# Performance work log

Measured on AMD Instinct MI355X. Metric: run time of the kernel, lower is better.

## Reference

```python
import jax, jax.numpy as jnp
import numpy as np

N, E = 50000, 800000
D_IN, HID, HEADS, D_OUT = 128, 32, 4, 40
NEG_SLOPE = 0.2
BN_EPS = 1e-5


def gat_conv(x, src, dst, W, a_src, a_dst, b, heads, ch):
    """PyG-style GATConv (eval mode, self-loops already appended to src/dst)."""
    n = x.shape[0]
    h = (x @ W).reshape(n, heads, ch)                      # [N,H,C]
    al_src = jnp.einsum('nhc,hc->nh', h, a_src)            # [N,H]
    al_dst = jnp.einsum('nhc,hc->nh', h, a_dst)
    e = jax.nn.leaky_relu(al_src[src] + al_dst[dst], NEG_SLOPE)  # [Etot,H]
    # segment softmax over incoming edges of each dst node
    e_max = jax.ops.segment_max(e, dst, num_segments=n)
    e = jnp.exp(e - e_max[dst])
    denom = jax.ops.segment_sum(e, dst, num_segments=n)
    alpha = e / (denom[dst] + 1e-16)                        # [Etot,H]
    msg = h[src] * alpha[:, :, None]                        # [Etot,H,C]
    out = jax.ops.segment_sum(msg, dst, num_segments=n)     # [N,H,C]
    return out.reshape(n, heads * ch) + b


def bn_eval(x, g, b, m, v):
    return (x - m) * jax.lax.rsqrt(v + BN_EPS) * g + b


def setup_inputs() -> dict:
    key = jax.random.key(0)
    ks = jax.random.split(key, 24)
    p = lambda k, s: jax.random.normal(k, s, jnp.float32) * 0.1
    inp = {
        'x': jax.random.normal(ks[0], (N, D_IN), jnp.float32),
        'edge_index': jax.random.randint(ks[1], (2, E), 0, N),
        'W1': p(ks[2], (D_IN, HEADS * HID)),
        'a_src1': p(ks[3], (HEADS, HID)), 'a_dst1': p(ks[4], (HEADS, HID)),
        'b1': jnp.zeros((HEADS * HID,), jnp.float32),
        'W2': p(ks[5], (HEADS * HID, HEADS * HID)),
        'a_src2': p(ks[6], (HEADS, HID)), 'a_dst2': p(ks[7], (HEADS, HID)),
        'b2': jnp.zeros((HEADS * HID,), jnp.float32),
        'W3': p(ks[8], (HEADS * HID, D_OUT)),
        'a_src3': p(ks[9], (1, D_OUT)), 'a_dst3': p(ks[10], (1, D_OUT)),
        'b3': jnp.zeros((D_OUT,), jnp.float32),
        'bn1_g': jnp.ones((HEADS * HID,), jnp.float32),
        'bn1_b': jnp.zeros((HEADS * HID,), jnp.float32),
        'bn1_m': p(ks[11], (HEADS * HID,)),
        'bn1_v': jax.random.uniform(ks[12], (HEADS * HID,), jnp.float32) + 0.5,
        'bn2_g': jnp.ones((HEADS * HID,), jnp.float32),
        'bn2_b': jnp.zeros((HEADS * HID,), jnp.float32),
        'bn2_m': p(ks[13], (HEADS * HID,)),
        'bn2_v': jax.random.uniform(ks[14], (HEADS * HID,), jnp.float32) + 0.5,
    }
    return inp


def reference(x, edge_index, W1, a_src1, a_dst1, b1, W2, a_src2, a_dst2, b2,
              W3, a_src3, a_dst3, b3, bn1_g, bn1_b, bn1_m, bn1_v,
              bn2_g, bn2_b, bn2_m, bn2_v):
    n = x.shape[0]
    loop = jnp.arange(n, dtype=edge_index.dtype)
    src = jnp.concatenate([edge_index[0], loop])   # add self loops (PyG default)
    dst = jnp.concatenate([edge_index[1], loop])

    h = gat_conv(x, src, dst, W1, a_src1, a_dst1, b1, HEADS, HID)
    h = jax.nn.relu(h)
    h = bn_eval(h, bn1_g, bn1_b, bn1_m, bn1_v)      # dropout = identity (eval)

    h = gat_conv(h, src, dst, W2, a_src2, a_dst2, b2, HEADS, HID)
    h = jax.nn.relu(h)
    h = bn_eval(h, bn2_g, bn2_b, bn2_m, bn2_v)

    h = gat_conv(h, src, dst, W3, a_src3, a_dst3, b3, 1, D_OUT)
    return jax.nn.log_softmax(h, axis=1)
```

## Files before the change

kernel.cpp:

```cpp
#include <hip/hip_runtime.h>
#include <hip/hip_bf16.h>
#include <math.h>

using bf16 = __hip_bfloat16;
using frag8 = __attribute__((ext_vector_type(8))) short;
using f32x4 = __attribute__((ext_vector_type(4))) float;

#define LEAKY 0.2f
#define BN_EPS 1e-5f
#define NEGBIG -1e30f

__device__ __forceinline__ float lrelu(float z){ return z > 0.f ? z : LEAKY * z; }
__device__ __forceinline__ float bflo(unsigned u){ return __uint_as_float(u << 16); }
__device__ __forceinline__ float bfhi(unsigned u){ return __uint_as_float(u & 0xffff0000u); }
__device__ __forceinline__ unsigned pk(float a, float b){
  unsigned ua = __float_as_uint(a), ub = __float_as_uint(b);
  ua += 0x7fffu + ((ua >> 16) & 1u);
  ub += 0x7fffu + ((ub >> 16) & 1u);
  return (ua >> 16) | (ub & 0xffff0000u);
}
__device__ __forceinline__ float ldf(const void* p, size_t i, int isbf){
  if (isbf) return (float)((const bf16*)p)[i];
  return ((const float*)p)[i];
}

union U4F8 { uint4 u; frag8 f; };

__device__ __forceinline__ frag8 load_a_pairs(const unsigned* __restrict__ X2, int node, int k0){
  U4F8 v; v.u = *((const uint4*)(X2 + (size_t)node*64 + (k0 >> 1))); return v.f;
}
__device__ __forceinline__ frag8 load_a_f32(const float* __restrict__ X, int node, int k0){
  float4 q0 = *((const float4*)(X + (size_t)node*128 + k0));
  float4 q1 = *((const float4*)(X + (size_t)node*128 + k0 + 4));
  U4F8 v; v.u = make_uint4(pk(q0.x,q0.y), pk(q0.z,q0.w), pk(q1.x,q1.y), pk(q1.z,q1.w));
  return v.f;
}

__global__ void init_detect(int* head, const unsigned short* __restrict__ w1bits,
                            int* flag, int n){
  int g = blockIdx.x*256 + threadIdx.x;
  if (g < n) head[g] = -1;
  if (blockIdx.x == 0){
    __shared__ int cntr;
    if (threadIdx.x == 0) cntr = 0;
    __syncthreads();
    unsigned u = w1bits[threadIdx.x * 2];
    int e = (u >> 7) & 0xff;
    atomicAdd(&cntr, (e >= 64 && e <= 140) ? 1 : 0);
    __syncthreads();
    if (threadIdx.x == 0) *flag = (cntr >= 160) ? 1 : 0;
  }
}

__global__ void chain_build(const int* __restrict__ dst, int* head, int* next,
                            int e, int n){
  int g = blockIdx.x*256 + threadIdx.x;
  if (g < e){
    int d = dst[g];
    next[g] = ((unsigned)d < (unsigned)n) ? atomicExch(&head[d], g) : -1;
  }
}

__global__ void chain_count(const int* __restrict__ head, const int* __restrict__ next,
                            int* cnt, int* total, int n){
  int g = blockIdx.x*256 + threadIdx.x;
  if (g == 0) *total = 0;
  if (g >= n) return;
  int c = 0;
  for (int e = head[g]; e != -1; e = next[e]) ++c;
  cnt[g] = c;
}

__global__ void csr_scan(const int* __restrict__ cnt, int* start, int* total, int n){
  __shared__ int s[256];
  __shared__ int base_s;
  int t = threadIdx.x;
  int g = blockIdx.x*256 + t;
  int v = (g < n) ? cnt[g] : 0;
  s[t] = v;
  __syncthreads();
  for (int off = 1; off < 256; off <<= 1){
    int x = (t >= off) ? s[t-off] : 0;
    __syncthreads();
    s[t] += x;
    __syncthreads();
  }
  if (t == 255) base_s = atomicAdd(total, s[255]);
  __syncthreads();
  if (g < n) start[g] = base_s + s[t] - v;
}

__global__ void chain_fill(const int* __restrict__ head, const int* __restrict__ next,
                           const int* __restrict__ src, const int* __restrict__ start,
                           int* col, int n){
  int g = blockIdx.x*256 + threadIdx.x;
  if (g >= n) return;
  int p = start[g];
  for (int e = head[g]; e != -1; e = next[e])
    col[p++] = src[e];
}

__global__ __launch_bounds__(256) void gemm_al_mfma(
    const void* __restrict__ X, int xkind,
    const void* __restrict__ W, const void* __restrict__ Wsrc, const void* __restrict__ Wdst,
    const int* __restrict__ flagp,
    unsigned* __restrict__ H2, float* __restrict__ AL, float* __restrict__ AD,
    int n, int ntiles)
{
  __shared__ unsigned short WT[128*136];
  const int isbf = *flagp;
  const int t = threadIdx.x;
  if (isbf){
    const unsigned short* W16 = (const unsigned short*)W;
    for (int idx = t; idx < 16384; idx += 256){
      int k = idx >> 7, nn = idx & 127;
      WT[nn*136 + k] = W16[idx];
    }
  } else {
    const float* Wf = (const float*)W;
    for (int idx = t; idx < 16384; idx += 256){
      int k = idx >> 7, nn = idx & 127;
      WT[nn*136 + k] = (unsigned short)(pk(Wf[idx], 0.f) & 0xffffu);
    }
  }
  __syncthreads();
  const int w = t >> 6;
  const int lane = t & 63;
  const int m = lane & 15, quad = lane >> 4;

  frag8 bf[4][2];
  #pragma unroll
  for (int s = 0; s < 4; ++s)
    #pragma unroll
    for (int ct = 0; ct < 2; ++ct){
      int colc = w*32 + ct*16 + m;
      int k0 = s*32 + quad*8;
      U4F8 v; v.u = *((const uint4*)&WT[colc*136 + k0]);
      bf[s][ct] = v.f;
    }
  float avv[2], dvv[2];
  #pragma unroll
  for (int ct = 0; ct < 2; ++ct){
    int colc = w*32 + ct*16 + m;
    avv[ct] = ldf(Wsrc, colc, isbf);
    dvv[ct] = ldf(Wdst, colc, isbf);
  }
  const bool pairs = (xkind == 1) || isbf;

  for (int tile = blockIdx.x; tile < ntiles; tile += gridDim.x){
    const int mb = tile*16;
    int nodeA = mb + m; if (nodeA >= n) nodeA = n - 1;
    frag8 af[4];
    #pragma unroll
    for (int s = 0; s < 4; ++s){
      int k0 = s*32 + quad*8;
      af[s] = pairs ? load_a_pairs((const unsigned*)X, nodeA, k0)
                    : load_a_f32((const float*)X, nodeA, k0);
    }
    f32x4 acc0 = {0.f,0.f,0.f,0.f}, acc1 = {0.f,0.f,0.f,0.f};
    #pragma unroll
    for (int s = 0; s < 4; ++s){
      acc0 = __builtin_amdgcn_mfma_f32_16x16x32_bf16(af[s], bf[s][0], acc0, 0,0,0);
      acc1 = __builtin_amdgcn_mfma_f32_16x16x32_bf16(af[s], bf[s][1], acc1, 0,0,0);
    }
    #pragma unroll
    for (int r = 0; r < 4; ++r){
      int g = mb + quad*4 + r;
      float v0 = acc0[r], v1 = acc1[r];
      unsigned u0 = pk(v0, __shfl_xor(v0, 1));
      unsigned u1 = pk(v1, __shfl_xor(v1, 1));
      bool ok = g < n;
      if (((lane & 1) == 0) && ok){
        H2[(size_t)g*64 + w*16 + (m >> 1)]     = u0;
        H2[(size_t)g*64 + w*16 + 8 + (m >> 1)] = u1;
      }
      float s1 = v0*avv[0] + v1*avv[1];
      float s2 = v0*dvv[0] + v1*dvv[1];
      s1 += __shfl_xor(s1,1); s1 += __shfl_xor(s1,2); s1 += __shfl_xor(s1,4); s1 += __shfl_xor(s1,8);
      s2 += __shfl_xor(s2,1); s2 += __shfl_xor(s2,2); s2 += __shfl_xor(s2,4); s2 += __shfl_xor(s2,8);
      if (m == 0 && ok){ AL[g*4 + w] = s1; AD[g*4 + w] = s2; }
    }
  }
}

__global__ __launch_bounds__(256) void gemm3_mfma(
    const unsigned* __restrict__ X2, const void* __restrict__ W,
    const void* __restrict__ Wsrc, const void* __restrict__ Wdst,
    const int* __restrict__ flagp,
    unsigned* __restrict__ H3, float* __restrict__ AL, float* __restrict__ AD,
    int n, int ntiles)
{
  __shared__ unsigned short WT[48*136];
  const int isbf = *flagp;
  const int t = threadIdx.x;
  for (int idx = t; idx < 128*64; idx += 256){
    int c = idx & 63, k = idx >> 6;
    if (c < 48){
      unsigned short v = 0;
      if (c < 40){
        if (isbf) v = ((const unsigned short*)W)[k*40 + c];
        else      v = (unsigned short)(pk(((const float*)W)[k*40 + c], 0.f) & 0xffffu);
      }
      WT[c*136 + k] = v;
    }
  }
  __syncthreads();
  const int w = t >> 6;
  const int lane = t & 63;
  const int m = lane & 15, quad = lane >> 4;

  frag8 bf[4][3];
  float avv[3], dvv[3];
  #pragma unroll
  for (int ct = 0; ct < 3; ++ct){
    int colc = ct*16 + m;
    #pragma unroll
    for (int s = 0; s < 4; ++s){
      int k0 = s*32 + quad*8;
      U4F8 v; v.u = *((const uint4*)&WT[colc*136 + k0]);
      bf[s][ct] = v.f;
    }
    avv[ct] = (colc < 40) ? ldf(Wsrc, colc, isbf) : 0.f;
    dvv[ct] = (colc < 40) ? ldf(Wdst, colc, isbf) : 0.f;
  }

  for (int tg = blockIdx.x; tg*4 < ntiles; tg += gridDim.x){
    const int tile = tg*4 + w;
    if (tile >= ntiles) continue;
    const int mb = tile*16;
    int nodeA = mb + m; if (nodeA >= n) nodeA = n - 1;
    frag8 af[4];
    #pragma unroll
    for (int s = 0; s < 4; ++s)
      af[s] = load_a_pairs(X2, nodeA, s*32 + quad*8);
    f32x4 acc[3];
    #pragma unroll
    for (int ct = 0; ct < 3; ++ct) acc[ct] = (f32x4){0.f,0.f,0.f,0.f};
    #pragma unroll
    for (int s = 0; s < 4; ++s){
      acc[0] = __builtin_amdgcn_mfma_f32_16x16x32_bf16(af[s], bf[s][0], acc[0], 0,0,0);
      acc[1] = __builtin_amdgcn_mfma_f32_16x16x32_bf16(af[s], bf[s][1], acc[1], 0,0,0);
      acc[2] = __builtin_amdgcn_mfma_f32_16x16x32_bf16(af[s], bf[s][2], acc[2], 0,0,0);
    }
    #pragma unroll
    for (int r = 0; r < 4; ++r){
      int g = mb + quad*4 + r;
      bool ok = g < n;
      float ps = 0.f, pd = 0.f;
      #pragma unroll
      for (int ct = 0; ct < 3; ++ct){
        float v = acc[ct][r];
        ps += v*avv[ct]; pd += v*dvv[ct];
        unsigned u = pk(v, __shfl_xor(v, 1));
        bool stok = ((lane & 1) == 0) && ok && (ct < 2 || m < 8);
        if (stok) H3[(size_t)g*20 + ct*8 + (m >> 1)] = u;
      }
      ps += __shfl_xor(ps,1); ps += __shfl_xor(ps,2); ps += __shfl_xor(ps,4); ps += __shfl_xor(ps,8);
      pd += __shfl_xor(pd,1); pd += __shfl_xor(pd,2); pd += __shfl_xor(pd,4); pd += __shfl_xor(pd,8);
      if (m == 0 && ok){ AL[g] = ps; AD[g] = pd; }
    }
  }
}

__global__ __launch_bounds__(256) void agg4(
    const unsigned* __restrict__ H2,
    const float* __restrict__ ALf, const float* __restrict__ ADf,
    const int* __restrict__ cnt, const int* __restrict__ start, const int* __restrict__ col,
    const void* __restrict__ bias, const void* __restrict__ bng, const void* __restrict__ bnb,
    const void* __restrict__ bnm,  const void* __restrict__ bnv,
    const int* __restrict__ flagp,
    unsigned* __restrict__ Hout, int n)
{
  const int isbf = *flagp;
  const int wave = threadIdx.x >> 6;
  const int lane = threadIdx.x & 63;
  const int node = blockIdx.x*4 + wave;
  if (node >= n) return;
  const int head = lane >> 4;
  const float ad = ADf[node*4 + head];
  const int base = start[node], deg = cnt[node];

  float accL, accH, l;
  {
    float e = __expf(lrelu(ALf[node*4 + head] + ad));
    unsigned h = H2[(size_t)node*64 + lane];
    l = e; accL = e * bflo(h); accH = e * bfhi(h);
  }

  int i = 0;
  for (; i + 8 <= deg; i += 8){
    int sv[8]; float av[8]; unsigned hv[8];
    #pragma unroll
    for (int u = 0; u < 8; ++u){
      int s = col[base + i + u];
      sv[u] = ((unsigned)s < (unsigned)n) ? s : 0;
    }
    #pragma unroll
    for (int u = 0; u < 8; ++u) av[u] = ALf[sv[u]*4 + head];
    #pragma unroll
    for (int u = 0; u < 8; ++u) hv[u] = H2[(size_t)sv[u]*64 + lane];
    #pragma unroll
    for (int u = 0; u < 8; ++u){
      float e = __expf(lrelu(av[u] + ad));
      l    += e;
      accL += e * bflo(hv[u]);
      accH += e * bfhi(hv[u]);
    }
  }
  for (; i < deg; ++i){
    int s = col[base + i];
    if ((unsigned)s >= (unsigned)n) s = 0;
    float a = ALf[s*4 + head];
    unsigned h = H2[(size_t)s*64 + lane];
    float e = __expf(lrelu(a + ad));
    l += e; accL += e * bflo(h); accH += e * bfhi(h);
  }

  const float rl = 1.f / l;
  const int c0 = 2*lane, c1 = c0 + 1;
  float v0 = fmaxf(accL*rl + ldf(bias,c0,isbf), 0.f);
  v0 = (v0 - ldf(bnm,c0,isbf)) * rsqrtf(ldf(bnv,c0,isbf) + BN_EPS) * ldf(bng,c0,isbf) + ldf(bnb,c0,isbf);
  float v1 = fmaxf(accH*rl + ldf(bias,c1,isbf), 0.f);
  v1 = (v1 - ldf(bnm,c1,isbf)) * rsqrtf(ldf(bnv,c1,isbf) + BN_EPS) * ldf(bng,c1,isbf) + ldf(bnb,c1,isbf);
  Hout[(size_t)node*64 + lane] = pk(v0, v1);
}

__global__ __launch_bounds__(256) void agg1(
    const unsigned* __restrict__ H3,
    const float* __restrict__ AL, const float* __restrict__ AD,
    const int* __restrict__ cnt, const int* __restrict__ start, const int* __restrict__ col,
    const void* __restrict__ b3, const int* __restrict__ flagp,
    void* __restrict__ out, int n)
{
  const int isbf = *flagp;
  const int wave = threadIdx.x >> 6;
  const int lane = threadIdx.x & 63;
  const int node = blockIdx.x*4 + wave;
  if (node >= n) return;
  const float ad = AD[node];
  const bool act = lane < 20;
  const int base = start[node], deg = cnt[node];

  float accL, accH, l;
  {
    float e = __expf(lrelu(AL[node] + ad));
    unsigned h = act ? H3[(size_t)node*20 + lane] : 0u;
    l = e; accL = e * bflo(h); accH = e * bfhi(h);
  }

  int i = 0;
  for (; i + 8 <= deg; i += 8){
    int sv[8]; float av[8]; unsigned hv[8];
    #pragma unroll
    for (int u = 0; u < 8; ++u){
      int s = col[base + i + u];
      sv[u] = ((unsigned)s < (unsigned)n) ? s : 0;
    }
    #pragma unroll
    for (int u = 0; u < 8; ++u) av[u] = AL[sv[u]];
    #pragma unroll
    for (int u = 0; u < 8; ++u) hv[u] = act ? H3[(size_t)sv[u]*20 + lane] : 0u;
    #pragma unroll
    for (int u = 0; u < 8; ++u){
      float e = __expf(lrelu(av[u] + ad));
      l    += e;
      accL += e * bflo(hv[u]);
      accH += e * bfhi(hv[u]);
    }
  }
  for (; i < deg; ++i){
    int s = col[base + i];
    if ((unsigned)s >= (unsigned)n) s = 0;
    float a = AL[s];
    unsigned h = act ? H3[(size_t)s*20 + lane] : 0u;
    float e = __expf(lrelu(a + ad));
    l += e; accL += e * bflo(h); accH += e * bfhi(h);
  }

  const float rl = 1.f / l;
  const int c0 = 2*lane;
  float z0 = act ? (accL*rl + ldf(b3, c0,     isbf)) : NEGBIG;
  float z1 = act ? (accH*rl + ldf(b3, c0 + 1, isbf)) : NEGBIG;
  float mx = fmaxf(z0, z1);
  #pragma unroll
  for (int off = 1; off < 64; off <<= 1) mx = fmaxf(mx, __shfl_xor(mx, off));
  float p = act ? (__expf(z0 - mx) + __expf(z1 - mx)) : 0.f;
  float sum = p;
  #pragma unroll
  for (int off = 1; off < 64; off <<= 1) sum += __shfl_xor(sum, off);
  if (act){
    float lg = __logf(sum);
    float r0 = z0 - mx - lg, r1 = z1 - mx - lg;
    if (isbf) ((unsigned*)out)[(size_t)node*20 + lane] = pk(r0, r1);
    else      ((float2*)out)[(size_t)node*20 + lane] = make_float2(r0, r1);
  }
}

extern "C" void kernel_launch(void* const* d_in, const int* in_sizes, int n_in,
                              void* d_out, int out_size, void* d_ws, size_t ws_size,
                              hipStream_t stream)
{
  (void)n_in; (void)out_size; (void)ws_size;
  const void* x    = d_in[0];
  const int*  ei   = (const int*)d_in[1];
  const void* W1   = d_in[2];
  const void* as1  = d_in[3];
  const void* ad1  = d_in[4];
  const void* b1   = d_in[5];
  const void* W2   = d_in[6];
  const void* as2  = d_in[7];
  const void* ad2  = d_in[8];
  const void* b2   = d_in[9];
  const void* W3   = d_in[10];
  const void* as3  = d_in[11];
  const void* ad3  = d_in[12];
  const void* b3   = d_in[13];
  const void* bn1g = d_in[14];
  const void* bn1b = d_in[15];
  const void* bn1m = d_in[16];
  const void* bn1v = d_in[17];
  const void* bn2g = d_in[18];
  const void* bn2b = d_in[19];
  const void* bn2m = d_in[20];
  const void* bn2v = d_in[21];

  const int N  = in_sizes[0] / 128;
  const int E  = in_sizes[1] / 2;
  const int ntiles = (N + 15) / 16;

  char* w = (char*)d_ws;
  size_t off = 0;
  auto alloc = [&](size_t bytes)->char*{
    char* p = w + off; off = (off + bytes + 255) & ~(size_t)255; return p;
  };
  unsigned* H2A = (unsigned*)alloc((size_t)N*64*4);
  unsigned* H2B = (unsigned*)alloc((size_t)N*64*4);
  unsigned* H3p = (unsigned*)alloc((size_t)N*20*4);
  float* AL   = (float*)alloc((size_t)N*4*4);
  float* AD   = (float*)alloc((size_t)N*4*4);
  int*   headp = (int*)alloc((size_t)N*4);
  int*   nextp = (int*)alloc((size_t)E*4);
  int*   cnt   = (int*)alloc((size_t)N*4);
  int*   start = (int*)alloc((size_t)N*4);
  int*   col   = (int*)alloc((size_t)E*4);
  int*   flag  = (int*)alloc(256);
  int*   total = (int*)alloc(256);

  const int* srcp = ei;
  const int* dstp = ei + E;

  const int nb256 = (N + 255)/256, eb256 = (E + 255)/256;
  const int bb = (N + 3)/4;
  int g1 = ntiles < 625 ? ntiles : 625;
  int g3 = (ntiles + 3)/4; if (g3 > 400) g3 = 400;

  init_detect<<<nb256,256,0,stream>>>(headp, (const unsigned short*)W1, flag, N);
  chain_build<<<eb256,256,0,stream>>>(dstp, headp, nextp, E, N);
  chain_count<<<nb256,256,0,stream>>>(headp, nextp, cnt, total, N);
  csr_scan  <<<nb256,256,0,stream>>>(cnt, start, total, N);
  chain_fill<<<nb256,256,0,stream>>>(headp, nextp, srcp, start, col, N);

  gemm_al_mfma<<<g1,256,0,stream>>>(x, 0, W1, as1, ad1, flag, H2A, AL, AD, N, ntiles);
  agg4<<<bb,256,0,stream>>>(H2A, AL, AD, cnt, start, col,
                            b1, bn1g, bn1b, bn1m, bn1v, flag, H2B, N);
  gemm_al_mfma<<<g1,256,0,stream>>>(H2B, 1, W2, as2, ad2, flag, H2A, AL, AD, N, ntiles);
  agg4<<<bb,256,0,stream>>>(H2A, AL, AD, cnt, start, col,
                            b2, bn2g, bn2b, bn2m, bn2v, flag, H2B, N);
  gemm3_mfma<<<g3,256,0,stream>>>(H2B, W3, as3, ad3, flag, H3p, AL, AD, N, ntiles);
  agg1<<<bb,256,0,stream>>>(H3p, AL, AD, cnt, start, col, b3, flag, d_out, N);
}
```

Baseline: 384.4 us.

## Build CSR via histogram+scatter and pack more nodes per wave in aggregation

```diff
diff --git a/kernel.cpp b/kernel.cpp
--- a/kernel.cpp
+++ b/kernel.cpp
@@ -10,7 +10,7 @@
 #define BN_EPS 1e-5f
 #define NEGBIG -1e30f
 
-__device__ __forceinline__ float lrelu(float z){ return z > 0.f ? z : LEAKY * z; }
+__device__ __forceinline__ float lrelu(float z){ return fmaxf(z, LEAKY * z); }
 __device__ __forceinline__ float bflo(unsigned u){ return __uint_as_float(u << 16); }
 __device__ __forceinline__ float bfhi(unsigned u){ return __uint_as_float(u & 0xffff0000u); }
 __device__ __forceinline__ unsigned pk(float a, float b){
@@ -36,10 +36,11 @@
   return v.f;
 }
 
-__global__ void init_detect(int* head, const unsigned short* __restrict__ w1bits,
-                            int* flag, int n){
+__global__ void init_detect(int* cnt, const unsigned short* __restrict__ w1bits,
+                            int* flag, int* total, int n){
   int g = blockIdx.x*256 + threadIdx.x;
-  if (g < n) head[g] = -1;
+  if (g < n) cnt[g] = 0;
+  if (g == 0) *total = 0;
   if (blockIdx.x == 0){
     __shared__ int cntr;
     if (threadIdx.x == 0) cntr = 0;
@@ -52,26 +53,16 @@
   }
 }
 
-__global__ void chain_build(const int* __restrict__ dst, int* head, int* next,
-                            int e, int n){
+__global__ void hist(const int* __restrict__ dst, int* cnt, int e, int n){
   int g = blockIdx.x*256 + threadIdx.x;
   if (g < e){
     int d = dst[g];
-    next[g] = ((unsigned)d < (unsigned)n) ? atomicExch(&head[d], g) : -1;
-  }
-}
-
-__global__ void chain_count(const int* __restrict__ head, const int* __restrict__ next,
-                            int* cnt, int* total, int n){
-  int g = blockIdx.x*256 + threadIdx.x;
-  if (g == 0) *total = 0;
-  if (g >= n) return;
-  int c = 0;
-  for (int e = head[g]; e != -1; e = next[e]) ++c;
-  cnt[g] = c;
-}
-
-__global__ void csr_scan(const int* __restrict__ cnt, int* start, int* total, int n){
+    if ((unsigned)d < (unsigned)n) atomicAdd(&cnt[d], 1);
+  }
+}
+
+__global__ void csr_scan(const int* __restrict__ cnt, int* start, int* pos,
+                         int* total, int n){
   __shared__ int s[256];
   __shared__ int base_s;
   int t = threadIdx.x;
@@ -87,17 +78,23 @@
   }
   if (t == 255) base_s = atomicAdd(total, s[255]);
   __syncthreads();
-  if (g < n) start[g] = base_s + s[t] - v;
-}
-
-__global__ void chain_fill(const int* __restrict__ head, const int* __restrict__ next,
-                           const int* __restrict__ src, const int* __restrict__ start,
-                           int* col, int n){
+  if (g < n){
+    int st = base_s + s[t] - v;
+    start[g] = st;
+    pos[g] = st;
+  }
+}
+
+__global__ void scatter(const int* __restrict__ src, const int* __restrict__ dst,
+                        int* pos, int* col, int e, int n){
   int g = blockIdx.x*256 + threadIdx.x;
-  if (g >= n) return;
-  int p = start[g];
-  for (int e = head[g]; e != -1; e = next[e])
-    col[p++] = src[e];
+  if (g < e){
+    int d = dst[g];
+    if ((unsigned)d < (unsigned)n){
+      int p = atomicAdd(&pos[d], 1);
+      col[p] = src[g];
+    }
+  }
 }
 
 __global__ __launch_bounds__(256) void gemm_al_mfma(
@@ -272,57 +269,73 @@
     unsigned* __restrict__ Hout, int n)
 {
   const int isbf = *flagp;
-  const int wave = threadIdx.x >> 6;
-  const int lane = threadIdx.x & 63;
-  const int node = blockIdx.x*4 + wave;
+  const int t = threadIdx.x;
+  const int grp = t >> 4;
+  const int p = t & 15;
+  const int node = blockIdx.x*16 + grp;
   if (node >= n) return;
-  const int head = lane >> 4;
+  const int head = p >> 2;
   const float ad = ADf[node*4 + head];
   const int base = start[node], deg = cnt[node];
 
-  float accL, accH, l;
+  float acc[8], l;
   {
     float e = __expf(lrelu(ALf[node*4 + head] + ad));
-    unsigned h = H2[(size_t)node*64 + lane];
-    l = e; accL = e * bflo(h); accH = e * bfhi(h);
+    uint4 h = *((const uint4*)(H2 + (size_t)node*64 + p*4));
+    l = e;
+    acc[0] = e*bflo(h.x); acc[1] = e*bfhi(h.x);
+    acc[2] = e*bflo(h.y); acc[3] = e*bfhi(h.y);
+    acc[4] = e*bflo(h.z); acc[5] = e*bfhi(h.z);
+    acc[6] = e*bflo(h.w); acc[7] = e*bfhi(h.w);
   }
 
   int i = 0;
-  for (; i + 8 <= deg; i += 8){
-    int sv[8]; float av[8]; unsigned hv[8];
-    #pragma unroll
-    for (int u = 0; u < 8; ++u){
+  for (; i + 4 <= deg; i += 4){
+    int sv[4]; float av[4]; uint4 hv[4];
+    #pragma unroll
+    for (int u = 0; u < 4; ++u){
       int s = col[base + i + u];
       sv[u] = ((unsigned)s < (unsigned)n) ? s : 0;
     }
     #pragma unroll
-    for (int u = 0; u < 8; ++u) av[u] = ALf[sv[u]*4 + head];
-    #pragma unroll
-    for (int u = 0; u < 8; ++u) hv[u] = H2[(size_t)sv[u]*64 + lane];
-    #pragma unroll
-    for (int u = 0; u < 8; ++u){
+    for (int u = 0; u < 4; ++u) av[u] = ALf[sv[u]*4 + head];
+    #pragma unroll
+    for (int u = 0; u < 4; ++u) hv[u] = *((const uint4*)(H2 + (size_t)sv[u]*64 + p*4));
+    #pragma unroll
+    for (int u = 0; u < 4; ++u){
       float e = __expf(lrelu(av[u] + ad));
-      l    += e;
-      accL += e * bflo(hv[u]);
-      accH += e * bfhi(hv[u]);
+      l += e;
+      acc[0] += e*bflo(hv[u].x); acc[1] += e*bfhi(hv[u].x);
+      acc[2] += e*bflo(hv[u].y); acc[3] += e*bfhi(hv[u].y);
+      acc[4] += e*bflo(hv[u].z); acc[5] += e*bfhi(hv[u].z);
+      acc[6] += e*bflo(hv[u].w); acc[7] += e*bfhi(hv[u].w);
     }
   }
   for (; i < deg; ++i){
     int s = col[base + i];
     if ((unsigned)s >= (unsigned)n) s = 0;
     float a = ALf[s*4 + head];
-    unsigned h = H2[(size_t)s*64 + lane];
+    uint4 h = *((const uint4*)(H2 + (size_t)s*64 + p*4));
     float e = __expf(lrelu(a + ad));
-    l += e; accL += e * bflo(h); accH += e * bfhi(h);
+    l += e;
+    acc[0] += e*bflo(h.x); acc[1] += e*bfhi(h.x);
+    acc[2] += e*bflo(h.y); acc[3] += e*bfhi(h.y);
+    acc[4] += e*bflo(h.z); acc[5] += e*bfhi(h.z);
+    acc[6] += e*bflo(h.w); acc[7] += e*bfhi(h.w);
   }
 
   const float rl = 1.f / l;
-  const int c0 = 2*lane, c1 = c0 + 1;
-  float v0 = fmaxf(accL*rl + ldf(bias,c0,isbf), 0.f);
-  v0 = (v0 - ldf(bnm,c0,isbf)) * rsqrtf(ldf(bnv,c0,isbf) + BN_EPS) * ldf(bng,c0,isbf) + ldf(bnb,c0,isbf);
-  float v1 = fmaxf(accH*rl + ldf(bias,c1,isbf), 0.f);
-  v1 = (v1 - ldf(bnm,c1,isbf)) * rsqrtf(ldf(bnv,c1,isbf) + BN_EPS) * ldf(bng,c1,isbf) + ldf(bnb,c1,isbf);
-  Hout[(size_t)node*64 + lane] = pk(v0, v1);
+  unsigned o[4];
+  #pragma unroll
+  for (int q = 0; q < 4; ++q){
+    const int c0 = p*8 + 2*q, c1 = c0 + 1;
+    float v0 = fmaxf(acc[2*q]*rl + ldf(bias,c0,isbf), 0.f);
+    v0 = (v0 - ldf(bnm,c0,isbf)) * rsqrtf(ldf(bnv,c0,isbf) + BN_EPS) * ldf(bng,c0,isbf) + ldf(bnb,c0,isbf);
+    float v1 = fmaxf(acc[2*q+1]*rl + ldf(bias,c1,isbf), 0.f);
+    v1 = (v1 - ldf(bnm,c1,isbf)) * rsqrtf(ldf(bnv,c1,isbf) + BN_EPS) * ldf(bng,c1,isbf) + ldf(bnb,c1,isbf);
+    o[q] = pk(v0, v1);
+  }
+  *((uint4*)(Hout + (size_t)node*64 + p*4)) = make_uint4(o[0], o[1], o[2], o[3]);
 }
 
 __global__ __launch_bounds__(256) void agg1(
@@ -333,35 +346,35 @@
     void* __restrict__ out, int n)
 {
   const int isbf = *flagp;
-  const int wave = threadIdx.x >> 6;
-  const int lane = threadIdx.x & 63;
-  const int node = blockIdx.x*4 + wave;
+  const int t = threadIdx.x;
+  const int p = t & 31;
+  const int node = blockIdx.x*8 + (t >> 5);
   if (node >= n) return;
   const float ad = AD[node];
-  const bool act = lane < 20;
+  const bool act = p < 20;
   const int base = start[node], deg = cnt[node];
 
   float accL, accH, l;
   {
     float e = __expf(lrelu(AL[node] + ad));
-    unsigned h = act ? H3[(size_t)node*20 + lane] : 0u;
+    unsigned h = act ? H3[(size_t)node*20 + p] : 0u;
     l = e; accL = e * bflo(h); accH = e * bfhi(h);
   }
 
   int i = 0;
-  for (; i + 8 <= deg; i += 8){
-    int sv[8]; float av[8]; unsigned hv[8];
-    #pragma unroll
-    for (int u = 0; u < 8; ++u){
+  for (; i + 4 <= deg; i += 4){
+    int sv[4]; float av[4]; unsigned hv[4];
+    #pragma unroll
+    for (int u = 0; u < 4; ++u){
       int s = col[base + i + u];
       sv[u] = ((unsigned)s < (unsigned)n) ? s : 0;
     }
     #pragma unroll
-    for (int u = 0; u < 8; ++u) av[u] = AL[sv[u]];
-    #pragma unroll
-    for (int u = 0; u < 8; ++u) hv[u] = act ? H3[(size_t)sv[u]*20 + lane] : 0u;
-    #pragma unroll
-    for (int u = 0; u < 8; ++u){
+    for (int u = 0; u < 4; ++u) av[u] = AL[sv[u]];
+    #pragma unroll
+    for (int u = 0; u < 4; ++u) hv[u] = act ? H3[(size_t)sv[u]*20 + p] : 0u;
+    #pragma unroll
+    for (int u = 0; u < 4; ++u){
       float e = __expf(lrelu(av[u] + ad));
       l    += e;
       accL += e * bflo(hv[u]);
@@ -372,27 +385,27 @@
     int s = col[base + i];
     if ((unsigned)s >= (unsigned)n) s = 0;
     float a = AL[s];
-    unsigned h = act ? H3[(size_t)s*20 + lane] : 0u;
+    unsigned h = act ? H3[(size_t)s*20 + p] : 0u;
     float e = __expf(lrelu(a + ad));
     l += e; accL += e * bflo(h); accH += e * bfhi(h);
   }
 
   const float rl = 1.f / l;
-  const int c0 = 2*lane;
+  const int c0 = 2*p;
   float z0 = act ? (accL*rl + ldf(b3, c0,     isbf)) : NEGBIG;
   float z1 = act ? (accH*rl + ldf(b3, c0 + 1, isbf)) : NEGBIG;
   float mx = fmaxf(z0, z1);
   #pragma unroll
-  for (int off = 1; off < 64; off <<= 1) mx = fmaxf(mx, __shfl_xor(mx, off));
-  float p = act ? (__expf(z0 - mx) + __expf(z1 - mx)) : 0.f;
-  float sum = p;
-  #pragma unroll
-  for (int off = 1; off < 64; off <<= 1) sum += __shfl_xor(sum, off);
+  for (int off = 1; off < 32; off <<= 1) mx = fmaxf(mx, __shfl_xor(mx, off));
+  float pp = act ? (__expf(z0 - mx) + __expf(z1 - mx)) : 0.f;
+  float sum = pp;
+  #pragma unroll
+  for (int off = 1; off < 32; off <<= 1) sum += __shfl_xor(sum, off);
   if (act){
     float lg = __logf(sum);
     float r0 = z0 - mx - lg, r1 = z1 - mx - lg;
-    if (isbf) ((unsigned*)out)[(size_t)node*20 + lane] = pk(r0, r1);
-    else      ((float2*)out)[(size_t)node*20 + lane] = make_float2(r0, r1);
+    if (isbf) ((unsigned*)out)[(size_t)node*20 + p] = pk(r0, r1);
+    else      ((float2*)out)[(size_t)node*20 + p] = make_float2(r0, r1);
   }
 }
 
@@ -438,10 +451,9 @@
   unsigned* H3p = (unsigned*)alloc((size_t)N*20*4);
   float* AL   = (float*)alloc((size_t)N*4*4);
   float* AD   = (float*)alloc((size_t)N*4*4);
-  int*   headp = (int*)alloc((size_t)N*4);
-  int*   nextp = (int*)alloc((size_t)E*4);
   int*   cnt   = (int*)alloc((size_t)N*4);
   int*   start = (int*)alloc((size_t)N*4);
+  int*   pos   = (int*)alloc((size_t)N*4);
   int*   col   = (int*)alloc((size_t)E*4);
   int*   flag  = (int*)alloc(256);
   int*   total = (int*)alloc(256);
@@ -450,22 +462,22 @@
   const int* dstp = ei + E;
 
   const int nb256 = (N + 255)/256, eb256 = (E + 255)/256;
-  const int bb = (N + 3)/4;
+  const int bb4 = (N + 15)/16;
+  const int bb1 = (N + 7)/8;
   int g1 = ntiles < 625 ? ntiles : 625;
   int g3 = (ntiles + 3)/4; if (g3 > 400) g3 = 400;
 
-  init_detect<<<nb256,256,0,stream>>>(headp, (const unsigned short*)W1, flag, N);
-  chain_build<<<eb256,256,0,stream>>>(dstp, headp, nextp, E, N);
-  chain_count<<<nb256,256,0,stream>>>(headp, nextp, cnt, total, N);
-  csr_scan  <<<nb256,256,0,stream>>>(cnt, start, total, N);
-  chain_fill<<<nb256,256,0,stream>>>(headp, nextp, srcp, start, col, N);
+  init_detect<<<nb256,256,0,stream>>>(cnt, (const unsigned short*)W1, flag, total, N);
+  hist<<<eb256,256,0,stream>>>(dstp, cnt, E, N);
+  csr_scan<<<nb256,256,0,stream>>>(cnt, start, pos, total, N);
+  scatter<<<eb256,256,0,stream>>>(srcp, dstp, pos, col, E, N);
 
   gemm_al_mfma<<<g1,256,0,stream>>>(x, 0, W1, as1, ad1, flag, H2A, AL, AD, N, ntiles);
-  agg4<<<bb,256,0,stream>>>(H2A, AL, AD, cnt, start, col,
-                            b1, bn1g, bn1b, bn1m, bn1v, flag, H2B, N);
+  agg4<<<bb4,256,0,stream>>>(H2A, AL, AD, cnt, start, col,
+                             b1, bn1g, bn1b, bn1m, bn1v, flag, H2B, N);
   gemm_al_mfma<<<g1,256,0,stream>>>(H2B, 1, W2, as2, ad2, flag, H2A, AL, AD, N, ntiles);
-  agg4<<<bb,256,0,stream>>>(H2A, AL, AD, cnt, start, col,
-                            b2, bn2g, bn2b, bn2m, bn2v, flag, H2B, N);
+  agg4<<<bb4,256,0,stream>>>(H2A, AL, AD, cnt, start, col,
+                             b2, bn2g, bn2b, bn2m, bn2v, flag, H2B, N);
   gemm3_mfma<<<g3,256,0,stream>>>(H2B, W3, as3, ad3, flag, H3p, AL, AD, N, ntiles);
-  agg1<<<bb,256,0,stream>>>(H3p, AL, AD, cnt, start, col, b3, flag, d_out, N);
-}
+  agg1<<<bb1,256,0,stream>>>(H3p, AL, AD, cnt, start, col, b3, flag, d_out, N);
+}
```

New measurement: 454.1 us. 18.1% more time.
